# Kernel optimization log

Hardware: AMD Instinct MI355X
Metric: run time of the kernel (lower is better)

The kernel has to match this reference:

```python
import jax, jax.numpy as jnp
import numpy as np
from jax import lax

K = 3          # local attention window (kernel_size)
DIL = 1        # dilation
PAD = DIL * (K - 1) // 2  # 'same' padding for the window gather


def _patches(t):
    # t: [B, C, H, W] -> [B, C, K*K, H, W] local neighborhoods (zero-padded)
    B, C, H, W = t.shape
    p = lax.conv_general_dilated_patches(
        t, filter_shape=(K, K), window_strides=(1, 1),
        padding=((PAD, PAD), (PAD, PAD)), rhs_dilation=(DIL, DIL))
    # output channels ordered (C, K, K) -> [B, C, K*K, H, W]
    return p.reshape(B, C, K * K, H, W)


def setup_inputs() -> dict:
    key = jax.random.key(0)
    k1, k2, k3, k4 = jax.random.split(key, 4)
    B, C, H, W = 4, 64, 256, 256
    x = jax.random.normal(k1, (B, C, H, W), dtype=jnp.float32)
    w_qkv = jax.random.normal(k2, (3 * C, C), dtype=jnp.float32) * 0.1
    b_qkv = jax.random.normal(k3, (3 * C,), dtype=jnp.float32) * 0.1
    w_mlp = jax.random.normal(k4, (C, C, K, K), dtype=jnp.float32) * 0.1
    return {"x": x, "w_qkv": w_qkv, "b_qkv": b_qkv, "w_mlp": w_mlp}


def reference(x, w_qkv, b_qkv, w_mlp):
    C = x.shape[1]
    scale = C ** (-0.5)
    # 1x1 qkv conv
    qkv = jnp.einsum('bchw,oc->bohw', x, w_qkv) + b_qkv[None, :, None, None]
    q, k, v = jnp.split(qkv, 3, axis=1)
    # conv1: local window QK^T -> [B, K*K, H, W]
    kp = _patches(k)                                   # [B,C,K*K,H,W]
    dots = jnp.einsum('bchw,bcnhw->bnhw', q, kp) * scale
    attn = jax.nn.softmax(dots, axis=1)                # softmax over window dim
    # conv2: attention-weighted aggregation of v neighbors -> [B,C,H,W]
    vp = _patches(v)
    out = jnp.einsum('bnhw,bcnhw->bchw', attn, vp)
    out = out + x                                      # residual
    # mlp: 3x3 conv, stride 1, padding 1, no bias
    out = lax.conv_general_dilated(out, w_mlp, (1, 1), ((PAD, PAD), (PAD, PAD)))
    return jax.nn.relu(out)
```

## Files before the change

### kernel.cpp

```cpp
#include <hip/hip_runtime.h>
#include <hip/hip_bf16.h>

typedef __attribute__((ext_vector_type(8))) short short8;
typedef __attribute__((ext_vector_type(4))) short short4_;
typedef __attribute__((ext_vector_type(4))) float float4_;
typedef __attribute__((ext_vector_type(4))) unsigned int uint4_;

#define CH 64
#define HH 256
#define WW 256
#define HW (HH*WW)
#define CHW (CH*HW)

#define TW 16
#define TH 8
#define XPW 20
#define XPH 12
#define NXP 240
#define OPW 18
#define OPH 10
#define NOP 180

#define XLS 72
#define KQ2 40
#define KQS 24
#define O1S 72
#define TSF 33

#define QB2_OFF 9600
#define O1_OFF  5760
#define SMEM_SHORTS 18720

#define WSQ_SHORTS 12288
#define WSM_SHORTS 36864

__device__ __forceinline__ float b2f(unsigned short u) {
    return __uint_as_float(((unsigned)u) << 16);
}
__device__ __forceinline__ float blo(unsigned u) {
    return __uint_as_float(u << 16);
}
__device__ __forceinline__ float bhi(unsigned u) {
    return __uint_as_float(u & 0xffff0000u);
}
__device__ __forceinline__ short f2bs(float f) {
    __hip_bfloat16 h = __float2bfloat16(f);
    short s; __builtin_memcpy(&s, &h, 2); return s;
}
__device__ __forceinline__ unsigned pack2(float a, float b) {
    return (unsigned)(unsigned short)f2bs(a) |
           ((unsigned)(unsigned short)f2bs(b) << 16);
}

__device__ __forceinline__ int xls_idx(int pix, int c) {
    int g = ((c >> 3) ^ ((pix >> 2) & 7));
    return pix * XLS + g * 8 + (c & 7);
}

#if defined(__has_builtin)
#if __has_builtin(__builtin_amdgcn_fdot2_f32_bf16)
#define HAS_BF16_DOT2 1
#endif
#endif
#ifdef HAS_BF16_DOT2
typedef __bf16 bf16x2 __attribute__((ext_vector_type(2)));
__device__ __forceinline__ float dot2acc(unsigned a, unsigned b, float acc) {
    return __builtin_amdgcn_fdot2_f32_bf16(__builtin_bit_cast(bf16x2, a),
                                           __builtin_bit_cast(bf16x2, b),
                                           acc, false);
}
#else
__device__ __forceinline__ float dot2acc(unsigned a, unsigned b, float acc) {
    acc += blo(a) * blo(b);
    acc += bhi(a) * bhi(b);
    return acc;
}
#endif

__global__ void prep_pack(const float* __restrict__ wqkv,
                          const float* __restrict__ wmlp,
                          short* __restrict__ wsq, short* __restrict__ wsm) {
    int idx = blockIdx.x * blockDim.x + threadIdx.x;
    int stride = gridDim.x * blockDim.x;
    for (int e = idx; e < WSQ_SHORTS; e += stride) {
        int j = e & 7, lane = (e >> 3) & 63;
        int ks = (e >> 9) & 1, q16 = (e >> 10) & 3, sec = e >> 12;
        int row = sec*64 + q16*16 + (lane & 15);
        int kk  = ks*32 + (lane >> 4)*8 + j;
        wsq[e] = f2bs(wqkv[(size_t)row*64 + kk]);
    }
    for (int e = idx; e < WSM_SHORTS; e += stride) {
        int j = e & 7, lane = (e >> 3) & 63;
        int rest = e >> 9;
        int nt = rest / 18, ks = rest % 18;
        int o   = nt*16 + (lane & 15);
        int cin = (ks & 1)*32 + (lane >> 4)*8 + j;
        int tap = ks >> 1;
        wsm[e] = f2bs(wmlp[(size_t)o*576 + cin*9 + tap]);
    }
}

__global__ __launch_bounds__(256, 3) void fused_mfma(
    const float* __restrict__ x, const short* __restrict__ wsq,
    const float* __restrict__ bqkv, const short* __restrict__ wsm,
    float* __restrict__ out)
{
    __shared__ __align__(16) short smem[SMEM_SHORTS];
    short* xls   = smem;
    short* kbuf2 = smem;
    short* qbuf2 = smem + QB2_OFF;
    short* kbufV = smem;
    short* o1b   = smem + O1_OFF;
    float* tbA   = (float*)smem;
    float* tbB   = (float*)smem + 4224;

    const int t    = threadIdx.x;
    const int w    = t >> 6;
    const int lane = t & 63;
    const int n16  = lane & 15;
    const int quad = lane >> 4;

    const int d   = blockIdx.x + (blockIdx.y << 4) + (blockIdx.z << 9);
    const int nn  = ((d & 7) << 8) | (d >> 3);
    const int b   = nn >> 9;
    const int rem = nn & 511;
    const int gy0 = (rem >> 4) * TH;
    const int gx0 = (rem & 15) * TW;
    const float* xb = x + (size_t)b * CHW;


    for (int slot = t; slot < 32*12*6; slot += 256) {
        int s6 = slot % 6, y = (slot / 6) % 12, c2 = slot / 72;
        int c  = c2 * 2;
        int gy = gy0 - 2 + y;
        int gxb = gx0 - 4 + s6*4;
        float v0[4], v1[4];
        bool gyok = (unsigned)gy < HH;
        if (gyok && gxb >= 0 && gxb + 3 < WW) {
            float4_ f0 = *(const float4_*)(xb + (size_t)c*HW + gy*WW + gxb);
            float4_ f1 = *(const float4_*)(xb + (size_t)(c+1)*HW + gy*WW + gxb);
            #pragma unroll
            for (int i = 0; i < 4; ++i) { v0[i] = f0[i]; v1[i] = f1[i]; }
        } else {
            #pragma unroll
            for (int i = 0; i < 4; ++i) {
                int gx = gxb + i;
                bool ok = gyok && (unsigned)gx < WW;
                v0[i] = ok ? xb[(size_t)c*HW + gy*WW + gx] : 0.f;
                v1[i] = ok ? xb[(size_t)(c+1)*HW + gy*WW + gx] : 0.f;
            }
        }
        #pragma unroll
        for (int i = 0; i < 4; ++i) {
            int pxc = s6*4 + i - 2;
            if ((unsigned)pxc < XPW)
                *(unsigned*)&xls[xls_idx(y*XPW + pxc, c)] = pack2(v0[i], v1[i]);
        }
    }
    __syncthreads();

    unsigned okbits = 0;
    #pragma unroll
    for (int i = 0; i < 4; ++i)
        #pragma unroll
        for (int r = 0; r < 4; ++r) {
            int p = (w*4 + i)*16 + quad*4 + r;
            if (p < NXP) {
                int gy = gy0 - 2 + p / XPW, gx = gx0 - 2 + p % XPW;
                if (((unsigned)gy < HH) && ((unsigned)gx < WW))
                    okbits |= 1u << (i*4 + r);
            }
        }

    short8 afr[4][2];
    #pragma unroll
    for (int i = 0; i < 4; ++i) {
        int p = (w*4 + i)*16 + n16;
        int pr = (p < NXP) ? p : 0;
        #pragma unroll
        for (int ks = 0; ks < 2; ++ks)
            afr[i][ks] = *(const short8*)&xls[xls_idx(pr, ks*32 + quad*8)];
    }
    const int op_py = t / OPW, op_px = t % OPW;
    const int ogy = gy0 - 1 + op_py, ogx = gx0 - 1 + op_px;
    const bool oin = (t < NOP) && ((unsigned)ogy < HH) && ((unsigned)ogx < WW);
    const int xpix = (op_py + 1)*XPW + (op_px + 1);
    short8 resi[8];
    if (t < NOP) {
        #pragma unroll
        for (int g = 0; g < 8; ++g)
            resi[g] = *(const short8*)&xls[xls_idx(xpix, g*8)];
    }
    __syncthreads();

    auto wload = [&](int sec, int q16, int ks) -> short8 {
        return *(const short8*)&wsq[(((sec*4 + q16)*2 + ks) << 9) + lane*8];
    };
    auto gemm_halo = [&](short8 b0, short8 b1, float bias,
                         short* dst, int stride, int coff) {
        #pragma unroll
        for (int i = 0; i < 4; ++i) {
            float4_ c = {0.f, 0.f, 0.f, 0.f};
            c = __builtin_amdgcn_mfma_f32_16x16x32_bf16(afr[i][0], b0, c, 0, 0, 0);
            c = __builtin_amdgcn_mfma_f32_16x16x32_bf16(afr[i][1], b1, c, 0, 0, 0);
            #pragma unroll
            for (int r = 0; r < 4; ++r) {
                int p = (w*4 + i)*16 + quad*4 + r;
                bool ok = (okbits >> (i*4 + r)) & 1u;
                if (p < NXP)
                    dst[p*stride + coff + n16] = ok ? f2bs(c[r] + bias) : (short)0;
            }
        }
    };
    auto gemm_q = [&](short8 b0, short8 b1, float bias, int coff) {
        #pragma unroll
        for (int i = 0; i < 4; ++i) {
            float4_ c = {0.f, 0.f, 0.f, 0.f};
            c = __builtin_amdgcn_mfma_f32_16x16x32_bf16(afr[i][0], b0, c, 0, 0, 0);
            c = __builtin_amdgcn_mfma_f32_16x16x32_bf16(afr[i][1], b1, c, 0, 0, 0);
            #pragma unroll
            for (int r = 0; r < 4; ++r) {
                int p = (w*4 + i)*16 + quad*4 + r;
                int py = p / XPW, px = p % XPW;
                if ((unsigned)(py - 1) < (unsigned)OPH &&
                    (unsigned)(px - 1) < (unsigned)OPW) {
                    int op = (py - 1)*OPW + (px - 1);
                    qbuf2[op*KQ2 + coff + n16] = f2bs(c[r] + bias);
                }
            }
        }
    };

    float dots[9];
    #pragma unroll
    for (int n2 = 0; n2 < 9; ++n2) dots[n2] = 0.f;

    short8 pw0 = wload(0,0,0), pw1 = wload(0,0,1);

    #pragma unroll
    for (int rr = 0; rr < 2; ++rr) {
        {
            short8 b0 = wload(0, 2*rr+1, 0), b1 = wload(0, 2*rr+1, 1);
            gemm_q(pw0, pw1, bqkv[(2*rr)*16 + n16], 0);
            gemm_q(b0,  b1,  bqkv[(2*rr+1)*16 + n16], 16);
            short8 c0 = wload(1, 2*rr,   0), c1 = wload(1, 2*rr,   1);
            short8 d0 = wload(1, 2*rr+1, 0), d1 = wload(1, 2*rr+1, 1);
            gemm_halo(c0, c1, bqkv[64 + (2*rr)*16 + n16],  kbuf2, KQ2, 0);
            gemm_halo(d0, d1, bqkv[64 + (2*rr+1)*16 + n16], kbuf2, KQ2, 16);
        }
        __syncthreads();
        if (rr == 0) { pw0 = wload(0, 2, 0); pw1 = wload(0, 2, 1); }
        else         { pw0 = wload(2, 0, 0); pw1 = wload(2, 0, 1); }
        if (oin) {
            uint4_ qa = *(const uint4_*)&qbuf2[t*KQ2];
            uint4_ qb = *(const uint4_*)&qbuf2[t*KQ2 + 8];
            uint4_ qc = *(const uint4_*)&qbuf2[t*KQ2 + 16];
            uint4_ qd = *(const uint4_*)&qbuf2[t*KQ2 + 24];
            #pragma unroll
            for (int n2 = 0; n2 < 9; ++n2) {
                int np = xpix + (n2/3 - 1)*XPW + (n2%3 - 1);
                uint4_ ka = *(const uint4_*)&kbuf2[np*KQ2];
                uint4_ kb = *(const uint4_*)&kbuf2[np*KQ2 + 8];
                uint4_ kc = *(const uint4_*)&kbuf2[np*KQ2 + 16];
                uint4_ kd = *(const uint4_*)&kbuf2[np*KQ2 + 24];
                float s = dots[n2];
                #pragma unroll
                for (int j = 0; j < 4; ++j) s = dot2acc(qa[j], ka[j], s);
                #pragma unroll
                for (int j = 0; j < 4; ++j) s = dot2acc(qb[j], kb[j], s);
                #pragma unroll
                for (int j = 0; j < 4; ++j) s = dot2acc(qc[j], kc[j], s);
                #pragma unroll
                for (int j = 0; j < 4; ++j) s = dot2acc(qd[j], kd[j], s);
                dots[n2] = s;
            }
        }
        __syncthreads();
    }

    float attn[9];
    if (oin) {
        float mx = -1e30f;
        #pragma unroll
        for (int n2 = 0; n2 < 9; ++n2) { dots[n2] *= 0.125f; mx = fmaxf(mx, dots[n2]); }
        float se = 0.f;
        #pragma unroll
        for (int n2 = 0; n2 < 9; ++n2) { attn[n2] = __expf(dots[n2] - mx); se += attn[n2]; }
        float inv = 1.f / se;
        #pragma unroll
        for (int n2 = 0; n2 < 9; ++n2) attn[n2] *= inv;
    }

    #pragma unroll
    for (int q16 = 0; q16 < 4; ++q16) {
        gemm_halo(pw0, pw1, bqkv[128 + q16*16 + n16], kbufV, KQS, 0);
        __syncthreads();
        if (q16 < 3) { pw0 = wload(2, q16+1, 0); pw1 = wload(2, q16+1, 1); }
        if (t < NOP) {
            short8 s0, s1;
            if (oin) {
                float o1[16];
                uint4_ r0 = __builtin_bit_cast(uint4_, resi[q16*2]);
                uint4_ r1 = __builtin_bit_cast(uint4_, resi[q16*2 + 1]);
                #pragma unroll
                for (int j = 0; j < 4; ++j) {
                    o1[2*j]     = blo(r0[j]); o1[2*j + 1]     = bhi(r0[j]);
                    o1[8 + 2*j] = blo(r1[j]); o1[8 + 2*j + 1] = bhi(r1[j]);
                }
                #pragma unroll
                for (int n2 = 0; n2 < 9; ++n2) {
                    float a = attn[n2];
                    int np = xpix + (n2/3 - 1)*XPW + (n2%3 - 1);
                    uint4_ va = *(const uint4_*)&kbufV[np*KQS];
                    uint4_ vb = *(const uint4_*)&kbufV[np*KQS + 8];
                    #pragma unroll
                    for (int j = 0; j < 4; ++j) {
                        o1[2*j]         += a * blo(va[j]);
                        o1[2*j + 1]     += a * bhi(va[j]);
                        o1[8 + 2*j]     += a * blo(vb[j]);
                        o1[8 + 2*j + 1] += a * bhi(vb[j]);
                    }
                }
                #pragma unroll
                for (int j = 0; j < 8; ++j) {
                    s0[j] = f2bs(o1[j]);
                    s1[j] = f2bs(o1[8 + j]);
                }
            } else {
                #pragma unroll
                for (int j = 0; j < 8; ++j) { s0[j] = 0; s1[j] = 0; }
            }
            *(short8*)&o1b[t*O1S + q16*16]     = s0;
            *(short8*)&o1b[t*O1S + q16*16 + 8] = s1;
        }
        __syncthreads();
    }

    float4_ acc[4][2];
    #pragma unroll
    for (int nt = 0; nt < 4; ++nt) {
        acc[nt][0] = (float4_){0.f,0.f,0.f,0.f};
        acc[nt][1] = (float4_){0.f,0.f,0.f,0.f};
    }
    const int mtc0 = w*2, mtc1 = w*2 + 1;
    for (int ks = 0; ks < 18; ++ks) {
        int tap = ks >> 1;
        int dy = tap/3 - 1, dx = tap%3 - 1;
        int cin0 = (ks & 1)*32 + quad*8;
        int pixA = (mtc0 + 1 + dy)*OPW + (n16 + 1 + dx);
        int pixB = (mtc1 + 1 + dy)*OPW + (n16 + 1 + dx);
        short8 a0 = *(const short8*)&o1b[pixA*O1S + cin0];
        short8 a1 = *(const short8*)&o1b[pixB*O1S + cin0];
        #pragma unroll
        for (int nt = 0; nt < 4; ++nt) {
            short8 bb = *(const short8*)&wsm[((nt*18 + ks) << 9) + lane*8];
            acc[nt][0] = __builtin_amdgcn_mfma_f32_16x16x32_bf16(a0, bb, acc[nt][0], 0, 0, 0);
            acc[nt][1] = __builtin_amdgcn_mfma_f32_16x16x32_bf16(a1, bb, acc[nt][1], 0, 0, 0);
        }
    }
    __syncthreads();

    #pragma unroll
    for (int ntl = 0; ntl < 2; ++ntl)
        #pragma unroll
        for (int r = 0; r < 4; ++r) {
            tbA[(mtc0*16 + quad*4 + r)*TSF + ntl*16 + n16] = fmaxf(acc[ntl][0][r], 0.f);
            tbA[(mtc1*16 + quad*4 + r)*TSF + ntl*16 + n16] = fmaxf(acc[ntl][1][r], 0.f);
        }
    __syncthreads();
    {
        int pl = t & 127, oh = t >> 7;
        int ty_ = pl >> 4, tx_ = pl & 15;
        float* op = out + (size_t)b*CHW + (size_t)(oh*16)*HW
                    + (size_t)(gy0 + ty_)*WW + (gx0 + tx_);
        #pragma unroll
        for (int ii = 0; ii < 16; ++ii)
            op[(size_t)ii*HW] = tbA[pl*TSF + oh*16 + ii];
    }
    #pragma unroll
    for (int ntl = 0; ntl < 2; ++ntl)
        #pragma unroll
        for (int r = 0; r < 4; ++r) {
            tbB[(mtc0*16 + quad*4 + r)*TSF + ntl*16 + n16] = fmaxf(acc[2+ntl][0][r], 0.f);
            tbB[(mtc1*16 + quad*4 + r)*TSF + ntl*16 + n16] = fmaxf(acc[2+ntl][1][r], 0.f);
        }
    __syncthreads();
    {
        int pl = t & 127, oh = t >> 7;
        int ty_ = pl >> 4, tx_ = pl & 15;
        float* op = out + (size_t)b*CHW + (size_t)(32 + oh*16)*HW
                    + (size_t)(gy0 + ty_)*WW + (gx0 + tx_);
        #pragma unroll
        for (int ii = 0; ii < 16; ++ii)
            op[(size_t)ii*HW] = tbB[pl*TSF + oh*16 + ii];
    }
}

extern "C" void kernel_launch(void* const* d_in, const int* in_sizes, int n_in,
                              void* d_out, int out_size, void* d_ws, size_t ws_size,
                              hipStream_t stream) {
    const float* x    = (const float*)d_in[0];
    const float* wqkv = (const float*)d_in[1];
    const float* bqkv = (const float*)d_in[2];
    const float* wmlp = (const float*)d_in[3];
    float* outp = (float*)d_out;

    short* wsq = (short*)d_ws;
    short* wsm = wsq + WSQ_SHORTS;

    prep_pack<<<128, 256, 0, stream>>>(wqkv, wmlp, wsq, wsm);

    dim3 grid(WW/TW, HH/TH, 4);
    fused_mfma<<<grid, 256, 0, stream>>>(x, wsq, bqkv, wsm, outp);
}
```

Baseline: 251.2 us.

## Swizzle V and O1 shared buffers, batch V GEMM by 32 channels, prefetch MLP weights

Computes V in 32-channel chunks instead of 16, which halves the number of V-GEMM/aggregation rounds and their barriers. The V buffer and the O1 buffer get XOR-swizzled layouts and O1 drops its padding, to reduce LDS bank conflicts. The 3x3 MLP loop double-buffers its weight loads from global memory one k-step ahead. The trade-offs are slightly more shared memory and more live registers, which could hurt occupancy at 3 blocks per SM.

```diff
diff --git a/kernel.cpp b/kernel.cpp
--- a/kernel.cpp
+++ b/kernel.cpp
@@ -23,13 +23,13 @@
 
 #define XLS 72
 #define KQ2 40
-#define KQS 24
-#define O1S 72
+#define VS  32
+#define O1S 64
 #define TSF 33
 
 #define QB2_OFF 9600
-#define O1_OFF  5760
-#define SMEM_SHORTS 18720
+#define O1_OFF  7680
+#define SMEM_SHORTS 19200
 
 #define WSQ_SHORTS 12288
 #define WSM_SHORTS 36864
@@ -55,6 +55,13 @@
 __device__ __forceinline__ int xls_idx(int pix, int c) {
     int g = ((c >> 3) ^ ((pix >> 2) & 7));
     return pix * XLS + g * 8 + (c & 7);
+}
+__device__ __forceinline__ int o1_idx(int pix, int c) {
+    int g = (((c >> 3) ^ pix) & 7);
+    return pix * O1S + g * 8 + (c & 7);
+}
+__device__ __forceinline__ int vswz(int p) {
+    return (p ^ (p >> 2)) & 3;
 }
 
 #if defined(__has_builtin)
@@ -109,7 +116,7 @@
     short* xls   = smem;
     short* kbuf2 = smem;
     short* qbuf2 = smem + QB2_OFF;
-    short* kbufV = smem;
+    short* vbuf  = smem;
     short* o1b   = smem + O1_OFF;
     float* tbA   = (float*)smem;
     float* tbB   = (float*)smem + 4224;
@@ -196,8 +203,7 @@
     auto wload = [&](int sec, int q16, int ks) -> short8 {
         return *(const short8*)&wsq[(((sec*4 + q16)*2 + ks) << 9) + lane*8];
     };
-    auto gemm_halo = [&](short8 b0, short8 b1, float bias,
-                         short* dst, int stride, int coff) {
+    auto gemm_k = [&](short8 b0, short8 b1, float bias, int coff) {
         #pragma unroll
         for (int i = 0; i < 4; ++i) {
             float4_ c = {0.f, 0.f, 0.f, 0.f};
@@ -208,7 +214,25 @@
                 int p = (w*4 + i)*16 + quad*4 + r;
                 bool ok = (okbits >> (i*4 + r)) & 1u;
                 if (p < NXP)
-                    dst[p*stride + coff + n16] = ok ? f2bs(c[r] + bias) : (short)0;
+                    kbuf2[p*KQ2 + coff + n16] = ok ? f2bs(c[r] + bias) : (short)0;
+            }
+        }
+    };
+    auto gemm_v = [&](short8 b0, short8 b1, float bias, int coff) {
+        #pragma unroll
+        for (int i = 0; i < 4; ++i) {
+            float4_ c = {0.f, 0.f, 0.f, 0.f};
+            c = __builtin_amdgcn_mfma_f32_16x16x32_bf16(afr[i][0], b0, c, 0, 0, 0);
+            c = __builtin_amdgcn_mfma_f32_16x16x32_bf16(afr[i][1], b1, c, 0, 0, 0);
+            #pragma unroll
+            for (int r = 0; r < 4; ++r) {
+                int p = (w*4 + i)*16 + quad*4 + r;
+                bool ok = (okbits >> (i*4 + r)) & 1u;
+                if (p < NXP) {
+                    int cc = coff + n16;
+                    int idx = p*VS + ((((cc >> 3) ^ vswz(p)) & 3) << 3) + (cc & 7);
+                    vbuf[idx] = ok ? f2bs(c[r] + bias) : (short)0;
+                }
             }
         }
     };
@@ -245,8 +269,8 @@
             gemm_q(b0,  b1,  bqkv[(2*rr+1)*16 + n16], 16);
             short8 c0 = wload(1, 2*rr,   0), c1 = wload(1, 2*rr,   1);
             short8 d0 = wload(1, 2*rr+1, 0), d1 = wload(1, 2*rr+1, 1);
-            gemm_halo(c0, c1, bqkv[64 + (2*rr)*16 + n16],  kbuf2, KQ2, 0);
-            gemm_halo(d0, d1, bqkv[64 + (2*rr+1)*16 + n16], kbuf2, KQ2, 16);
+            gemm_k(c0, c1, bqkv[64 + (2*rr)*16 + n16],  0);
+            gemm_k(d0, d1, bqkv[64 + (2*rr+1)*16 + n16], 16);
         }
         __syncthreads();
         if (rr == 0) { pw0 = wload(0, 2, 0); pw1 = wload(0, 2, 1); }
@@ -292,46 +316,55 @@
     }
 
     #pragma unroll
-    for (int q16 = 0; q16 < 4; ++q16) {
-        gemm_halo(pw0, pw1, bqkv[128 + q16*16 + n16], kbufV, KQS, 0);
+    for (int rr2 = 0; rr2 < 2; ++rr2) {
+        {
+            short8 b2 = wload(2, 2*rr2+1, 0), b3 = wload(2, 2*rr2+1, 1);
+            gemm_v(pw0, pw1, bqkv[128 + (2*rr2)*16 + n16], 0);
+            gemm_v(b2,  b3,  bqkv[128 + (2*rr2+1)*16 + n16], 16);
+        }
         __syncthreads();
-        if (q16 < 3) { pw0 = wload(2, q16+1, 0); pw1 = wload(2, q16+1, 1); }
+        if (rr2 == 0) { pw0 = wload(2, 2, 0); pw1 = wload(2, 2, 1); }
         if (t < NOP) {
-            short8 s0, s1;
-            if (oin) {
-                float o1[16];
-                uint4_ r0 = __builtin_bit_cast(uint4_, resi[q16*2]);
-                uint4_ r1 = __builtin_bit_cast(uint4_, resi[q16*2 + 1]);
-                #pragma unroll
-                for (int j = 0; j < 4; ++j) {
-                    o1[2*j]     = blo(r0[j]); o1[2*j + 1]     = bhi(r0[j]);
-                    o1[8 + 2*j] = blo(r1[j]); o1[8 + 2*j + 1] = bhi(r1[j]);
-                }
-                #pragma unroll
-                for (int n2 = 0; n2 < 9; ++n2) {
-                    float a = attn[n2];
-                    int np = xpix + (n2/3 - 1)*XPW + (n2%3 - 1);
-                    uint4_ va = *(const uint4_*)&kbufV[np*KQS];
-                    uint4_ vb = *(const uint4_*)&kbufV[np*KQS + 8];
+            #pragma unroll
+            for (int h2 = 0; h2 < 2; ++h2) {
+                const int kg = rr2*2 + h2;
+                short8 s0, s1;
+                if (oin) {
+                    float o1[16];
+                    uint4_ r0 = __builtin_bit_cast(uint4_, resi[kg*2]);
+                    uint4_ r1 = __builtin_bit_cast(uint4_, resi[kg*2 + 1]);
                     #pragma unroll
                     for (int j = 0; j < 4; ++j) {
-                        o1[2*j]         += a * blo(va[j]);
-                        o1[2*j + 1]     += a * bhi(va[j]);
-                        o1[8 + 2*j]     += a * blo(vb[j]);
-                        o1[8 + 2*j + 1] += a * bhi(vb[j]);
+                        o1[2*j]     = blo(r0[j]); o1[2*j + 1]     = bhi(r0[j]);
+                        o1[8 + 2*j] = blo(r1[j]); o1[8 + 2*j + 1] = bhi(r1[j]);
                     }
+                    #pragma unroll
+                    for (int n2 = 0; n2 < 9; ++n2) {
+                        float a = attn[n2];
+                        int np = xpix + (n2/3 - 1)*XPW + (n2%3 - 1);
+                        int sw = vswz(np);
+                        uint4_ va = *(const uint4_*)&vbuf[np*VS + (((h2*2)   ^ sw) << 3)];
+                        uint4_ vb = *(const uint4_*)&vbuf[np*VS + (((h2*2+1) ^ sw) << 3)];
+                        #pragma unroll
+                        for (int j = 0; j < 4; ++j) {
+                            o1[2*j]         += a * blo(va[j]);
+                            o1[2*j + 1]     += a * bhi(va[j]);
+                            o1[8 + 2*j]     += a * blo(vb[j]);
+                            o1[8 + 2*j + 1] += a * bhi(vb[j]);
+                        }
+                    }
+                    #pragma unroll
+                    for (int j = 0; j < 8; ++j) {
+                        s0[j] = f2bs(o1[j]);
+                        s1[j] = f2bs(o1[8 + j]);
+                    }
+                } else {
+                    #pragma unroll
+                    for (int j = 0; j < 8; ++j) { s0[j] = 0; s1[j] = 0; }
                 }
-                #pragma unroll
-                for (int j = 0; j < 8; ++j) {
-                    s0[j] = f2bs(o1[j]);
-                    s1[j] = f2bs(o1[8 + j]);
-                }
-            } else {
-                #pragma unroll
-                for (int j = 0; j < 8; ++j) { s0[j] = 0; s1[j] = 0; }
-            }
-            *(short8*)&o1b[t*O1S + q16*16]     = s0;
-            *(short8*)&o1b[t*O1S + q16*16 + 8] = s1;
+                *(short8*)&o1b[o1_idx(t, kg*16)]     = s0;
+                *(short8*)&o1b[o1_idx(t, kg*16 + 8)] = s1;
+            }
         }
         __syncthreads();
     }
@@ -343,20 +376,30 @@
         acc[nt][1] = (float4_){0.f,0.f,0.f,0.f};
     }
     const int mtc0 = w*2, mtc1 = w*2 + 1;
+    short8 cw[4], nw[4];
+    #pragma unroll
+    for (int nt = 0; nt < 4; ++nt)
+        cw[nt] = *(const short8*)&wsm[((nt*18 + 0) << 9) + lane*8];
     for (int ks = 0; ks < 18; ++ks) {
+        if (ks < 17) {
+            #pragma unroll
+            for (int nt = 0; nt < 4; ++nt)
+                nw[nt] = *(const short8*)&wsm[((nt*18 + ks + 1) << 9) + lane*8];
+        }
         int tap = ks >> 1;
         int dy = tap/3 - 1, dx = tap%3 - 1;
         int cin0 = (ks & 1)*32 + quad*8;
         int pixA = (mtc0 + 1 + dy)*OPW + (n16 + 1 + dx);
         int pixB = (mtc1 + 1 + dy)*OPW + (n16 + 1 + dx);
-        short8 a0 = *(const short8*)&o1b[pixA*O1S + cin0];
-        short8 a1 = *(const short8*)&o1b[pixB*O1S + cin0];
+        short8 a0 = *(const short8*)&o1b[o1_idx(pixA, cin0)];
+        short8 a1 = *(const short8*)&o1b[o1_idx(pixB, cin0)];
         #pragma unroll
         for (int nt = 0; nt < 4; ++nt) {
-            short8 bb = *(const short8*)&wsm[((nt*18 + ks) << 9) + lane*8];
-            acc[nt][0] = __builtin_amdgcn_mfma_f32_16x16x32_bf16(a0, bb, acc[nt][0], 0, 0, 0);
-            acc[nt][1] = __builtin_amdgcn_mfma_f32_16x16x32_bf16(a1, bb, acc[nt][1], 0, 0, 0);
-        }
+            acc[nt][0] = __builtin_amdgcn_mfma_f32_16x16x32_bf16(a0, cw[nt], acc[nt][0], 0, 0, 0);
+            acc[nt][1] = __builtin_amdgcn_mfma_f32_16x16x32_bf16(a1, cw[nt], acc[nt][1], 0, 0, 0);
+        }
+        #pragma unroll
+        for (int nt = 0; nt < 4; ++nt) cw[nt] = nw[nt];
     }
     __syncthreads();
 
```

Result: no change. 249.3 us (-0.8%).

## Replace padded LDS strides with XOR-swizzled layouts for K, Q, V and o1 buffers

Applied to the files above, without the earlier changes.

Drops the padded shared-memory strides (72/40/24) in favour of dense strides (64/32/16). Bank conflicts on the K/Q dot-product reads, the V aggregation reads and the o1 MFMA operand loads are instead avoided with XOR swizzles on the 8-element group index. This shrinks the per-block LDS footprint, which could allow more resident blocks if registers permit. V now gets its own swizzled buffer, and the two output staging halves share one buffer, which costs an extra block-wide barrier between them.

```diff
diff --git a/kernel.cpp b/kernel.cpp
--- a/kernel.cpp
+++ b/kernel.cpp
@@ -21,15 +21,15 @@
 #define OPH 10
 #define NOP 180
 
-#define XLS 72
-#define KQ2 40
-#define KQS 24
-#define O1S 72
+#define XLS 64
+#define KQS2 32
+#define VSS 16
+#define O1S 64
 #define TSF 33
 
-#define QB2_OFF 9600
-#define O1_OFF  5760
-#define SMEM_SHORTS 18720
+#define QB2_OFF 7680
+#define O1_OFF  3840
+#define SMEM_SHORTS 15360
 
 #define WSQ_SHORTS 12288
 #define WSM_SHORTS 36864
@@ -55,6 +55,17 @@
 __device__ __forceinline__ int xls_idx(int pix, int c) {
     int g = ((c >> 3) ^ ((pix >> 2) & 7));
     return pix * XLS + g * 8 + (c & 7);
+}
+__device__ __forceinline__ int kqswz(int p) {
+    return (p ^ (p >> 2)) & 3;
+}
+__device__ __forceinline__ int o1_idx(int pix, int c) {
+    int g = (((c >> 3) ^ pix) & 7);
+    return pix * O1S + g * 8 + (c & 7);
+}
+__device__ __forceinline__ int v_idx(int p, int c) {
+    int g = (((c >> 3) ^ p ^ (p >> 2)) & 1);
+    return p * VSS + g * 8 + (c & 7);
 }
 
 #if defined(__has_builtin)
@@ -109,10 +120,9 @@
     short* xls   = smem;
     short* kbuf2 = smem;
     short* qbuf2 = smem + QB2_OFF;
-    short* kbufV = smem;
+    short* vbuf  = smem;
     short* o1b   = smem + O1_OFF;
-    float* tbA   = (float*)smem;
-    float* tbB   = (float*)smem + 4224;
+    float* tbuf  = (float*)smem;
 
     const int t    = threadIdx.x;
     const int w    = t >> 6;
@@ -196,8 +206,7 @@
     auto wload = [&](int sec, int q16, int ks) -> short8 {
         return *(const short8*)&wsq[(((sec*4 + q16)*2 + ks) << 9) + lane*8];
     };
-    auto gemm_halo = [&](short8 b0, short8 b1, float bias,
-                         short* dst, int stride, int coff) {
+    auto gemm_k = [&](short8 b0, short8 b1, float bias, int coff) {
         #pragma unroll
         for (int i = 0; i < 4; ++i) {
             float4_ c = {0.f, 0.f, 0.f, 0.f};
@@ -207,8 +216,26 @@
             for (int r = 0; r < 4; ++r) {
                 int p = (w*4 + i)*16 + quad*4 + r;
                 bool ok = (okbits >> (i*4 + r)) & 1u;
+                if (p < NXP) {
+                    int cc = coff + n16;
+                    int idx = p*KQS2 + ((((cc >> 3) ^ kqswz(p)) & 3) << 3) + (cc & 7);
+                    kbuf2[idx] = ok ? f2bs(c[r] + bias) : (short)0;
+                }
+            }
+        }
+    };
+    auto gemm_v = [&](short8 b0, short8 b1, float bias) {
+        #pragma unroll
+        for (int i = 0; i < 4; ++i) {
+            float4_ c = {0.f, 0.f, 0.f, 0.f};
+            c = __builtin_amdgcn_mfma_f32_16x16x32_bf16(afr[i][0], b0, c, 0, 0, 0);
+            c = __builtin_amdgcn_mfma_f32_16x16x32_bf16(afr[i][1], b1, c, 0, 0, 0);
+            #pragma unroll
+            for (int r = 0; r < 4; ++r) {
+                int p = (w*4 + i)*16 + quad*4 + r;
+                bool ok = (okbits >> (i*4 + r)) & 1u;
                 if (p < NXP)
-                    dst[p*stride + coff + n16] = ok ? f2bs(c[r] + bias) : (short)0;
+                    vbuf[v_idx(p, n16)] = ok ? f2bs(c[r] + bias) : (short)0;
             }
         }
     };
@@ -225,7 +252,9 @@
                 if ((unsigned)(py - 1) < (unsigned)OPH &&
                     (unsigned)(px - 1) < (unsigned)OPW) {
                     int op = (py - 1)*OPW + (px - 1);
-                    qbuf2[op*KQ2 + coff + n16] = f2bs(c[r] + bias);
+                    int cc = coff + n16;
+                    int idx = op*KQS2 + ((((cc >> 3) ^ kqswz(op)) & 3) << 3) + (cc & 7);
+                    qbuf2[idx] = f2bs(c[r] + bias);
                 }
             }
         }
@@ -245,24 +274,26 @@
             gemm_q(b0,  b1,  bqkv[(2*rr+1)*16 + n16], 16);
             short8 c0 = wload(1, 2*rr,   0), c1 = wload(1, 2*rr,   1);
             short8 d0 = wload(1, 2*rr+1, 0), d1 = wload(1, 2*rr+1, 1);
-            gemm_halo(c0, c1, bqkv[64 + (2*rr)*16 + n16],  kbuf2, KQ2, 0);
-            gemm_halo(d0, d1, bqkv[64 + (2*rr+1)*16 + n16], kbuf2, KQ2, 16);
+            gemm_k(c0, c1, bqkv[64 + (2*rr)*16 + n16],  0);
+            gemm_k(d0, d1, bqkv[64 + (2*rr+1)*16 + n16], 16);
         }
         __syncthreads();
         if (rr == 0) { pw0 = wload(0, 2, 0); pw1 = wload(0, 2, 1); }
         else         { pw0 = wload(2, 0, 0); pw1 = wload(2, 0, 1); }
         if (oin) {
-            uint4_ qa = *(const uint4_*)&qbuf2[t*KQ2];
-            uint4_ qb = *(const uint4_*)&qbuf2[t*KQ2 + 8];
-            uint4_ qc = *(const uint4_*)&qbuf2[t*KQ2 + 16];
-            uint4_ qd = *(const uint4_*)&qbuf2[t*KQ2 + 24];
+            int swq = kqswz(t);
+            uint4_ qa = *(const uint4_*)&qbuf2[t*KQS2 + ((0^swq)<<3)];
+            uint4_ qb = *(const uint4_*)&qbuf2[t*KQS2 + ((1^swq)<<3)];
+            uint4_ qc = *(const uint4_*)&qbuf2[t*KQS2 + ((2^swq)<<3)];
+            uint4_ qd = *(const uint4_*)&qbuf2[t*KQS2 + ((3^swq)<<3)];
             #pragma unroll
             for (int n2 = 0; n2 < 9; ++n2) {
                 int np = xpix + (n2/3 - 1)*XPW + (n2%3 - 1);
-                uint4_ ka = *(const uint4_*)&kbuf2[np*KQ2];
-                uint4_ kb = *(const uint4_*)&kbuf2[np*KQ2 + 8];
-                uint4_ kc = *(const uint4_*)&kbuf2[np*KQ2 + 16];
-                uint4_ kd = *(const uint4_*)&kbuf2[np*KQ2 + 24];
+                int swk = kqswz(np);
+                uint4_ ka = *(const uint4_*)&kbuf2[np*KQS2 + ((0^swk)<<3)];
+                uint4_ kb = *(const uint4_*)&kbuf2[np*KQS2 + ((1^swk)<<3)];
+                uint4_ kc = *(const uint4_*)&kbuf2[np*KQS2 + ((2^swk)<<3)];
+                uint4_ kd = *(const uint4_*)&kbuf2[np*KQS2 + ((3^swk)<<3)];
                 float s = dots[n2];
                 #pragma unroll
                 for (int j = 0; j < 4; ++j) s = dot2acc(qa[j], ka[j], s);
@@ -293,7 +324,7 @@
 
     #pragma unroll
     for (int q16 = 0; q16 < 4; ++q16) {
-        gemm_halo(pw0, pw1, bqkv[128 + q16*16 + n16], kbufV, KQS, 0);
+        gemm_v(pw0, pw1, bqkv[128 + q16*16 + n16]);
         __syncthreads();
         if (q16 < 3) { pw0 = wload(2, q16+1, 0); pw1 = wload(2, q16+1, 1); }
         if (t < NOP) {
@@ -311,8 +342,9 @@
                 for (int n2 = 0; n2 < 9; ++n2) {
                     float a = attn[n2];
                     int np = xpix + (n2/3 - 1)*XPW + (n2%3 - 1);
-                    uint4_ va = *(const uint4_*)&kbufV[np*KQS];
-                    uint4_ vb = *(const uint4_*)&kbufV[np*KQS + 8];
+                    int sw = (np ^ (np >> 2)) & 1;
+                    uint4_ va = *(const uint4_*)&vbuf[np*VSS + ((0^sw)<<3)];
+                    uint4_ vb = *(const uint4_*)&vbuf[np*VSS + ((1^sw)<<3)];
                     #pragma unroll
                     for (int j = 0; j < 4; ++j) {
                         o1[2*j]         += a * blo(va[j]);
@@ -330,8 +362,8 @@
                 #pragma unroll
                 for (int j = 0; j < 8; ++j) { s0[j] = 0; s1[j] = 0; }
             }
-            *(short8*)&o1b[t*O1S + q16*16]     = s0;
-            *(short8*)&o1b[t*O1S + q16*16 + 8] = s1;
+            *(short8*)&o1b[o1_idx(t, q16*16)]     = s0;
+            *(short8*)&o1b[o1_idx(t, q16*16 + 8)] = s1;
         }
         __syncthreads();
     }
@@ -349,8 +381,8 @@
         int cin0 = (ks & 1)*32 + quad*8;
         int pixA = (mtc0 + 1 + dy)*OPW + (n16 + 1 + dx);
         int pixB = (mtc1 + 1 + dy)*OPW + (n16 + 1 + dx);
-        short8 a0 = *(const short8*)&o1b[pixA*O1S + cin0];
-        short8 a1 = *(const short8*)&o1b[pixB*O1S + cin0];
+        short8 a0 = *(const short8*)&o1b[o1_idx(pixA, cin0)];
+        short8 a1 = *(const short8*)&o1b[o1_idx(pixB, cin0)];
         #pragma unroll
         for (int nt = 0; nt < 4; ++nt) {
             short8 bb = *(const short8*)&wsm[((nt*18 + ks) << 9) + lane*8];
@@ -361,38 +393,27 @@
     __syncthreads();
 
     #pragma unroll
-    for (int ntl = 0; ntl < 2; ++ntl)
-        #pragma unroll
-        for (int r = 0; r < 4; ++r) {
-            tbA[(mtc0*16 + quad*4 + r)*TSF + ntl*16 + n16] = fmaxf(acc[ntl][0][r], 0.f);
-            tbA[(mtc1*16 + quad*4 + r)*TSF + ntl*16 + n16] = fmaxf(acc[ntl][1][r], 0.f);
-        }
-    __syncthreads();
-    {
-        int pl = t & 127, oh = t >> 7;
-        int ty_ = pl >> 4, tx_ = pl & 15;
-        float* op = out + (size_t)b*CHW + (size_t)(oh*16)*HW
-                    + (size_t)(gy0 + ty_)*WW + (gx0 + tx_);
-        #pragma unroll
-        for (int ii = 0; ii < 16; ++ii)
-            op[(size_t)ii*HW] = tbA[pl*TSF + oh*16 + ii];
-    }
-    #pragma unroll
-    for (int ntl = 0; ntl < 2; ++ntl)
-        #pragma unroll
-        for (int r = 0; r < 4; ++r) {
-            tbB[(mtc0*16 + quad*4 + r)*TSF + ntl*16 + n16] = fmaxf(acc[2+ntl][0][r], 0.f);
-            tbB[(mtc1*16 + quad*4 + r)*TSF + ntl*16 + n16] = fmaxf(acc[2+ntl][1][r], 0.f);
-        }
-    __syncthreads();
-    {
-        int pl = t & 127, oh = t >> 7;
-        int ty_ = pl >> 4, tx_ = pl & 15;
-        float* op = out + (size_t)b*CHW + (size_t)(32 + oh*16)*HW
-                    + (size_t)(gy0 + ty_)*WW + (gx0 + tx_);
-        #pragma unroll
-        for (int ii = 0; ii < 16; ++ii)
-            op[(size_t)ii*HW] = tbB[pl*TSF + oh*16 + ii];
+    for (int half = 0; half < 2; ++half) {
+        if (half) __syncthreads();
+        #pragma unroll
+        for (int ntl = 0; ntl < 2; ++ntl) {
+            int nt = half*2 + ntl;
+            #pragma unroll
+            for (int r = 0; r < 4; ++r) {
+                tbuf[(mtc0*16 + quad*4 + r)*TSF + ntl*16 + n16] = fmaxf(acc[nt][0][r], 0.f);
+                tbuf[(mtc1*16 + quad*4 + r)*TSF + ntl*16 + n16] = fmaxf(acc[nt][1][r], 0.f);
+            }
+        }
+        __syncthreads();
+        {
+            int pl = t & 127, oh = t >> 7;
+            int ty_ = pl >> 4, tx_ = pl & 15;
+            float* op = out + (size_t)b*CHW + (size_t)(half*32 + oh*16)*HW
+                        + (size_t)(gy0 + ty_)*WW + (gx0 + tx_);
+            #pragma unroll
+            for (int ii = 0; ii < 16; ++ii)
+                op[(size_t)ii*HW] = tbuf[pl*TSF + oh*16 + ii];
+        }
     }
 }
 
```

Result: slower. 306.4 us (+22.0%).
